# Kernel tuning notes

Hardware: AMD Instinct MI355X
Metric: run time of the kernel (lower is better)

Reference implementation:

```python
import jax, jax.numpy as jnp
from jax import lax
import numpy as np


def conv2d(x, w, b=None, stride=1, pad=0, groups=1):
    out = lax.conv_general_dilated(x, w, (stride, stride), [(pad, pad), (pad, pad)],
                                   dimension_numbers=('NCHW', 'OIHW', 'NCHW'),
                                   feature_group_count=groups)
    if b is not None:
        out = out + b[None, :, None, None]
    return out


def ln(x, g, b, eps=1e-5):
    m = x.mean(-1, keepdims=True)
    v = ((x - m) ** 2).mean(-1, keepdims=True)
    return (x - m) * lax.rsqrt(v + eps) * g + b


def grid_sample_bilinear(img, grid):
    # img [N,C,H,W]; grid [N,Hg,Wg,2] with (x,y) in [-1,1]; align_corners=True, zeros padding
    N, C, H, W = img.shape
    x = (grid[..., 0] + 1.0) * 0.5 * (W - 1)
    y = (grid[..., 1] + 1.0) * 0.5 * (H - 1)
    x0 = jnp.floor(x); y0 = jnp.floor(y)
    x1 = x0 + 1.0; y1 = y0 + 1.0
    wx1 = x - x0; wx0 = 1.0 - wx1
    wy1 = y - y0; wy0 = 1.0 - wy1
    imgh = img.transpose(0, 2, 3, 1)  # [N,H,W,C]
    bidx = jnp.arange(N)[:, None, None]
    def g(ix, iy):
        valid = (ix >= 0) & (ix <= W - 1) & (iy >= 0) & (iy <= H - 1)
        ixc = jnp.clip(ix, 0, W - 1).astype(jnp.int32)
        iyc = jnp.clip(iy, 0, H - 1).astype(jnp.int32)
        return imgh[bidx, iyc, ixc] * valid[..., None].astype(img.dtype)
    out = (g(x0, y0) * (wx0 * wy0)[..., None] + g(x1, y0) * (wx1 * wy0)[..., None]
           + g(x0, y1) * (wx0 * wy1)[..., None] + g(x1, y1) * (wx1 * wy1)[..., None])
    return out.transpose(0, 3, 1, 2)  # [N,C,Hg,Wg]


def setup_inputs() -> dict:
    key = jax.random.key(0)
    ks = iter(jax.random.split(key, 64))
    def rn(shape, s=0.02):
        return jax.random.normal(next(ks), shape, jnp.float32) * s
    B, C, H, W = 4, 512, 32, 32
    gc, hid = 256, 1024
    d = {}
    d['feat_tgt'] = jax.random.normal(next(ks), (B, C, H, W), jnp.float32)
    d['feat_ref'] = jax.random.normal(next(ks), (B, C, H, W), jnp.float32)
    d['emb_w'] = rn((C, 2 * C, 3, 3)); d['emb_b'] = jnp.zeros((C,), jnp.float32)
    d['q_w'] = rn((C, C)); d['q_b'] = jnp.zeros((C,), jnp.float32)
    d['k_w'] = rn((C, C)); d['k_b'] = jnp.zeros((C,), jnp.float32)
    d['v_w'] = rn((C, C)); d['v_b'] = jnp.zeros((C,), jnp.float32)
    d['out_w'] = rn((C, C)); d['out_b'] = jnp.zeros((C,), jnp.float32)
    d['ln1_w'] = jnp.ones((gc,), jnp.float32); d['ln1_b'] = jnp.zeros((gc,), jnp.float32)
    d['mb_n1_w'] = jnp.ones((gc,), jnp.float32); d['mb_n1_b'] = jnp.zeros((gc,), jnp.float32)
    d['mb_q_w'] = rn((gc, gc)); d['mb_q_b'] = jnp.zeros((gc,), jnp.float32)
    d['mb_kv_w'] = rn((2 * gc, gc)); d['mb_kv_b'] = jnp.zeros((2 * gc,), jnp.float32)
    d['mb_proj_w'] = rn((gc, gc)); d['mb_proj_b'] = jnp.zeros((gc,), jnp.float32)
    d['mb_n2_w'] = jnp.ones((gc,), jnp.float32); d['mb_n2_b'] = jnp.zeros((gc,), jnp.float32)
    d['mb_fc1_w'] = rn((hid, gc)); d['mb_fc1_b'] = jnp.zeros((hid,), jnp.float32)
    d['mb_dw_w'] = rn((hid, 1, 3, 3)); d['mb_dw_b'] = jnp.zeros((hid,), jnp.float32)
    d['mb_fc2_w'] = rn((gc, hid)); d['mb_fc2_b'] = jnp.zeros((gc,), jnp.float32)
    d['co_dw_w'] = rn((gc, 1, 9, 9)); d['co_dw_b'] = jnp.zeros((gc,), jnp.float32)
    d['co_ln_w'] = jnp.ones((gc,), jnp.float32); d['co_ln_b'] = jnp.zeros((gc,), jnp.float32)
    d['co_out_w'] = rn((2, gc))
    return d


def reference(feat_tgt, feat_ref, emb_w, emb_b, q_w, q_b, k_w, k_b, v_w, v_b, out_w, out_b,
              ln1_w, ln1_b, mb_n1_w, mb_n1_b, mb_q_w, mb_q_b, mb_kv_w, mb_kv_b,
              mb_proj_w, mb_proj_b, mb_n2_w, mb_n2_b, mb_fc1_w, mb_fc1_b, mb_dw_w, mb_dw_b,
              mb_fc2_w, mb_fc2_b, co_dw_w, co_dw_b, co_ln_w, co_ln_b, co_out_w):
    B, C, H, W = feat_tgt.shape
    G = 2                      # n_groups
    gc = C // G                # n_group_channels
    heads, hc = 8, C // 8      # n_heads, n_head_channels
    # embedding conv over concat(target, reference)
    feat = conv2d(jnp.concatenate([feat_tgt, feat_ref], 1), emb_w, emb_b, pad=1)
    q = jnp.einsum('bchw,oc->bohw', feat_tgt, q_w) + q_b[None, :, None, None]
    # group tokens + LN
    fg = feat.reshape(B * G, gc, H * W).transpose(0, 2, 1)  # [BG, N, gc]
    x = ln(fg, ln1_w, ln1_b)
    # ---- MitBlock offset generator ----
    BG, N, D = x.shape
    mh = 8; mhd = D // mh
    h = ln(x, mb_n1_w, mb_n1_b, 1e-6)
    qq = (h @ mb_q_w.T + mb_q_b).reshape(BG, N, mh, mhd).transpose(0, 2, 1, 3)
    kv = (h @ mb_kv_w.T + mb_kv_b).reshape(BG, N, 2, mh, mhd).transpose(2, 0, 3, 1, 4)
    kk, vv = kv[0], kv[1]
    a = jax.nn.softmax(jnp.einsum('bhnd,bhmd->bhnm', qq, kk) * (mhd ** -0.5), axis=-1)
    o = jnp.einsum('bhnm,bhmd->bhnd', a, vv).transpose(0, 2, 1, 3).reshape(BG, N, D)
    x = x + (o @ mb_proj_w.T + mb_proj_b)
    h2 = ln(x, mb_n2_w, mb_n2_b, 1e-6)
    m = h2 @ mb_fc1_w.T + mb_fc1_b                         # [BG, N, hid]
    hid = m.shape[-1]
    mi = m.transpose(0, 2, 1).reshape(BG, hid, H, W)
    mi = conv2d(mi, mb_dw_w, mb_dw_b, pad=1, groups=hid)
    m = jax.nn.gelu(mi.reshape(BG, hid, N).transpose(0, 2, 1), approximate=False)
    x = x + (m @ mb_fc2_w.T + mb_fc2_b)
    # ---- conv_offset stack ----
    off = x.reshape(BG, H, W, gc).transpose(0, 3, 1, 2)
    off = conv2d(off, co_dw_w, co_dw_b, pad=4, groups=gc)
    off = ln(off.transpose(0, 2, 3, 1), co_ln_w, co_ln_b).transpose(0, 3, 1, 2)
    off = jax.nn.gelu(off, approximate=False)
    off = jnp.einsum('bchw,oc->bohw', off, co_out_w)       # [BG, 2, Hk, Wk]
    Hk, Wk = off.shape[2], off.shape[3]
    ns = Hk * Wk
    rng = jnp.array([1.0 / Hk, 1.0 / Wk], feat.dtype).reshape(1, 2, 1, 1)
    off = jnp.tanh(off) * rng * 2.0                        # offset_range_factor = 2
    off = off.transpose(0, 2, 3, 1)                        # [BG, Hk, Wk, 2] (y,x)
    ry = (jnp.linspace(0.5, Hk - 0.5, Hk, dtype=feat.dtype) / Hk) * 2 - 1
    rx = (jnp.linspace(0.5, Wk - 0.5, Wk, dtype=feat.dtype) / Wk) * 2 - 1
    ref = jnp.stack(jnp.meshgrid(ry, rx, indexing='ij'), -1)  # [Hk, Wk, 2] (y,x)
    pos = off + ref[None]
    sampled = grid_sample_bilinear(feat.reshape(BG, gc, H, W), pos[..., ::-1])
    sampled = sampled.reshape(B, C, ns)
    k = jnp.einsum('bcn,oc->bon', sampled, k_w) + k_b[None, :, None]
    v = jnp.einsum('bcn,oc->bon', sampled, v_w) + v_b[None, :, None]
    qh = q.reshape(B * heads, hc, H * W)
    kh = k.reshape(B * heads, hc, ns)
    vh = v.reshape(B * heads, hc, ns)
    attn = jax.nn.softmax(jnp.einsum('bcm,bcn->bmn', qh, kh) * (hc ** -0.5), axis=-1)
    out = jnp.einsum('bmn,bcn->bcm', attn, vh).reshape(B, C, H, W)
    y = jnp.einsum('bchw,oc->bohw', out, out_w) + out_b[None, :, None, None]
    return y
```

## Files before the change

### kernel.cpp

```cpp
#include <hip/hip_runtime.h>
#include <math.h>


static constexpr int HW = 1024;

typedef __attribute__((ext_vector_type(8))) short bf16x8;
typedef __attribute__((ext_vector_type(4))) float f32x4;

union V16u { int4 i4; ushort u[8]; };

__device__ __forceinline__ float gelu_exact(float v) {
  return 0.5f * v * (1.0f + erff(v * 0.7071067811865475f));
}

__device__ __forceinline__ ushort bf16_rne(float v) {
  unsigned int b = __float_as_uint(v);
  return (ushort)((b + 0x7fffu + ((b >> 16) & 1u)) >> 16);
}

__device__ __forceinline__ void split2(float v, ushort& h, ushort& l) {
  h = bf16_rne(v);
  l = bf16_rne(v - __uint_as_float(((unsigned int)h) << 16));
}

__device__ __forceinline__ void wfrag_body(const float* __restrict__ W, int K, int KC,
                                           ushort* __restrict__ dh, ushort* __restrict__ dl,
                                           int gtid, float scale) {
  int l = gtid & 63; int fr = gtid >> 6;
  int kc = fr % KC; int ot = fr / KC;
  int lr = l & 15, lu = l >> 4;
  const float* sp = W + (size_t)(ot * 16 + lr) * K + kc * 32 + lu * 8;
  V16u hi, lo;
#pragma unroll
  for (int j = 0; j < 8; ++j) split2(sp[j] * scale, hi.u[j], lo.u[j]);
  *(int4*)(dh + (size_t)gtid * 8) = hi.i4;
  *(int4*)(dl + (size_t)gtid * 8) = lo.i4;
}

__global__ void k_prep_all(
    const float* __restrict__ emb_w, const float* __restrict__ tgt,
    const float* __restrict__ refp,
    const float* q_w, const float* k_w, const float* v_w, const float* o_w,
    const float* mq_w, const float* mkv_w, const float* mp_w,
    const float* f1_w, const float* f2_w, const float* dw9_w,
    const float* q_b, const float* mq_b, const float* mkv_b,
    const float* k_b, const float* v_b,
    ushort* __restrict__ WtEH, ushort* __restrict__ WtEL,
    ushort* __restrict__ XtH, ushort* __restrict__ XtL,
    ushort* qh, ushort* ql, ushort* kvh, ushort* kvl,
    ushort* oh, ushort* ol, ushort* mqkvh, ushort* mqkvl,
    ushort* mph, ushort* mpl, ushort* f1h, ushort* f1l, ushort* f2h, ushort* f2l,
    float* wt9, float* biasmb, float* biaskv, float* biasq,
    ushort* tgtfh, ushort* tgtfl) {
  int bid = blockIdx.x, tid = threadIdx.x;
  if (bid < 2048) {
    int idx = bid * 256 + tid;
    int o = idx >> 10, ci = idx & 1023;
    const float* src = emb_w + (size_t)idx * 9;
#pragma unroll
    for (int t = 0; t < 9; ++t) {
      ushort h, l; split2(src[t], h, l);
      size_t oo = ((size_t)(t * 512 + o)) * 1024 + ci;
      WtEH[oo] = h; WtEL[oo] = l;
    }
  } else if (bid < 4360) {
    int idx = (bid - 2048) * 256 + tid;
    int xp = idx % 34; int r = idx / 34;
    int g8 = r & 127; r >>= 7;
    int yp = r % 34; int b = r / 34;
    int y = yp - 1, x = xp - 1;
    bool valid = (unsigned)y < 32u && (unsigned)x < 32u;
    V16u hi, lo;
    const float* in = (g8 < 64) ? (tgt + ((size_t)(b * 512 + g8 * 8)) * HW)
                                : (refp + ((size_t)(b * 512 + (g8 - 64) * 8)) * HW);
#pragma unroll
    for (int j = 0; j < 8; ++j) {
      float v = valid ? in[(size_t)j * HW + y * 32 + x] : 0.f;
      split2(v, hi.u[j], lo.u[j]);
    }
    size_t oo = (((size_t)(b * 34 + yp)) * 34 + xp) * 1024 + g8 * 8;
    *(int4*)(XtH + oo) = hi.i4;
    *(int4*)(XtL + oo) = lo.i4;
  }
  else if (bid < 4488) wfrag_body(q_w, 512, 16, qh, ql, (bid - 4360) * 256 + tid, 0.125f);
  else if (bid < 4616) wfrag_body(k_w, 512, 16, kvh, kvl, (bid - 4488) * 256 + tid, 1.f);
  else if (bid < 4744) wfrag_body(v_w, 512, 16, kvh + 262144, kvl + 262144,
                                  (bid - 4616) * 256 + tid, 1.f);
  else if (bid < 4872) wfrag_body(o_w, 512, 16, oh, ol, (bid - 4744) * 256 + tid, 1.f);
  else if (bid < 4904) wfrag_body(mq_w, 256, 8, mqkvh, mqkvl, (bid - 4872) * 256 + tid,
                                  0.17677669529663689f);
  else if (bid < 4968) wfrag_body(mkv_w, 256, 8, mqkvh + 65536, mqkvl + 65536,
                                  (bid - 4904) * 256 + tid, 1.f);
  else if (bid < 5000) wfrag_body(mp_w, 256, 8, mph, mpl, (bid - 4968) * 256 + tid, 1.f);
  else if (bid < 5128) wfrag_body(f1_w, 256, 8, f1h, f1l, (bid - 5000) * 256 + tid, 1.f);
  else if (bid < 5256) wfrag_body(f2_w, 1024, 32, f2h, f2l, (bid - 5128) * 256 + tid, 1.f);
  else if (bid < 5337) {
    int idx = (bid - 5256) * 256 + tid;
    int t = idx >> 8, c = idx & 255;
    wt9[idx] = dw9_w[c * 81 + t];
  } else if (bid < 5346) {
    int idx = (bid - 5337) * 256 + tid;
    if (idx < 768)
      biasmb[idx] = idx < 256 ? mq_b[idx] * 0.17677669529663689f : mkv_b[idx - 256];
    else if (idx < 1792) {
      int j = idx - 768;
      biaskv[j] = j < 512 ? k_b[j] : v_b[j - 512];
    } else if (idx < 2304) {
      biasq[idx - 1792] = q_b[idx - 1792] * 0.125f;
    }
  } else {
    int gtid = (bid - 5346) * 256 + tid;
    int l = gtid & 63; int fr = gtid >> 6;
    int kc = fr % 16; int r2 = fr / 16; int nt = r2 & 63; int b = r2 >> 6;
    int lr = l & 15, lu = l >> 4;
    const float* sp = tgt + ((size_t)(b * 512) + kc * 32 + lu * 8) * 1024 + nt * 16 + lr;
    V16u hi, lo;
#pragma unroll
    for (int j = 0; j < 8; ++j) split2(sp[(size_t)j * 1024], hi.u[j], lo.u[j]);
    *(int4*)(tgtfh + (size_t)gtid * 8) = hi.i4;
    *(int4*)(tgtfl + (size_t)gtid * 8) = lo.i4;
  }
}

__global__ __launch_bounds__(256, 4)
void k_emb_mfma(const ushort* __restrict__ Xt_hi, const ushort* __restrict__ Xt_lo,
                const ushort* __restrict__ Wt_hi, const ushort* __restrict__ Wt_lo,
                float* __restrict__ part) {
  int wgid = (blockIdx.x & 7) * 128 + (blockIdx.x >> 3);
  int yt = wgid & 7;  wgid >>= 3;
  int b  = wgid & 3;  wgid >>= 2;
  int ks = wgid & 3;  wgid >>= 2;
  int mt = wgid;
  int tid = threadIdx.x;
  int w = tid >> 6, l = tid & 63;
  int lr = l & 15, lu = l >> 4;
  int y0 = yt * 4;
  int obase = mt * 64 + w * 16;

  __shared__ int4 LsH[816];
  __shared__ int4 LsL[816];

  int4 gh[4], gl[4];
  int kc0 = ks * 8;

  auto loadstage = [&](int kcg) {
#pragma unroll
    for (int i = 0; i < 4; ++i) {
      int s = tid + 256 * i;
      if (s < 816) {
        int px = s >> 2;
        int u = (s & 3) ^ ((px >> 1) & 3);
        size_t off = ((size_t)(b * 34 + y0) * 34 + px) * 1024 + kcg * 32 + u * 8;
        gh[i] = *(const int4*)(Xt_hi + off);
        gl[i] = *(const int4*)(Xt_lo + off);
      }
    }
  };
  auto writestage = [&]() {
#pragma unroll
    for (int i = 0; i < 4; ++i) {
      int s = tid + 256 * i;
      if (s < 816) { LsH[s] = gh[i]; LsL[s] = gl[i]; }
    }
  };

  f32x4 zero = {0.f, 0.f, 0.f, 0.f};
  f32x4 acc[8];
#pragma unroll
  for (int n = 0; n < 8; ++n) acc[n] = zero;

  loadstage(kc0);
  writestage();

  for (int kc = 0; kc < 8; ++kc) {
    __syncthreads();
    if (kc < 7) loadstage(kc0 + kc + 1);
    int kcg = kc0 + kc;
    const bf16x8* BH = (const bf16x8*)&LsH[0];
    const bf16x8* BL = (const bf16x8*)&LsL[0];
#pragma unroll
    for (int kx = 0; kx < 3; ++kx) {
      bf16x8 bh[12], bl[12];
#pragma unroll
      for (int f = 0; f < 12; ++f) {
        int px = (f >> 1) * 34 + (f & 1) * 16 + kx + lr;
        int idx = px * 4 + (lu ^ ((px >> 1) & 3));
        bh[f] = BH[idx]; bl[f] = BL[idx];
      }
#pragma unroll
      for (int ky = 0; ky < 3; ++ky) {
        int tap = ky * 3 + kx;
        size_t wo = (((size_t)(tap * 512 + obase + lr)) * 1024) + kcg * 32 + lu * 8;
        bf16x8 ah = *(const bf16x8*)(Wt_hi + wo);
        bf16x8 al = *(const bf16x8*)(Wt_lo + wo);
#pragma unroll
        for (int yr = 0; yr < 4; ++yr)
#pragma unroll
          for (int h = 0; h < 2; ++h) {
            int f = (yr + ky) * 2 + h;
            int nf = yr * 2 + h;
            acc[nf] = __builtin_amdgcn_mfma_f32_16x16x32_bf16(ah, bh[f], acc[nf], 0, 0, 0);
            acc[nf] = __builtin_amdgcn_mfma_f32_16x16x32_bf16(ah, bl[f], acc[nf], 0, 0, 0);
            acc[nf] = __builtin_amdgcn_mfma_f32_16x16x32_bf16(al, bh[f], acc[nf], 0, 0, 0);
          }
      }
    }
    if (kc < 7) {
      __syncthreads();
      writestage();
    }
  }

  float* pb = part + (size_t)ks * 2097152;
#pragma unroll
  for (int yr = 0; yr < 4; ++yr)
#pragma unroll
    for (int h = 0; h < 2; ++h) {
      f32x4 c = acc[yr * 2 + h];
      size_t base = ((size_t)(b * 512 + obase + lu * 4)) * 1024
                    + (y0 + yr) * 32 + h * 16 + lr;
#pragma unroll
      for (int r = 0; r < 4; ++r) pb[base + (size_t)r * 1024] = c[r];
    }
}

__global__ void k_embmerge_nc(const float* __restrict__ part, const float* __restrict__ bias,
                              float* __restrict__ featnc) {
  __shared__ float T[64][65];
  int bid = blockIdx.x;
  int n0 = (bid & 15) << 6; bid >>= 4;
  int c0 = (bid & 3) << 6; int bg = bid >> 2;
  int cl = threadIdx.x & 63, rw = threadIdx.x >> 6;
#pragma unroll
  for (int i = 0; i < 16; ++i) {
    int crow = i * 4 + rw;
    size_t idx = ((size_t)(bg * 256 + c0 + crow)) * 1024 + n0 + cl;
    float v = part[idx] + part[2097152 + idx] + part[4194304 + idx] + part[6291456 + idx];
    T[crow][cl] = v + bias[(bg & 1) * 256 + c0 + crow];
  }
  __syncthreads();
#pragma unroll
  for (int i = 0; i < 16; ++i) {
    int nrow = i * 4 + rw;
    featnc[((size_t)(bg * 1024 + n0 + nrow)) * 256 + c0 + cl] = T[cl][nrow];
  }
}

__global__ __launch_bounds__(256)
void k_gemm_mfma(const ushort* __restrict__ Ah, const ushort* __restrict__ Al,
                 const ushort* __restrict__ Bh, const ushort* __restrict__ Bl,
                 const float* __restrict__ bias, float* __restrict__ Y,
                 int KC, int MT, int Mtot) {
  int bid = blockIdx.x;
  int ntb = bid & 15; bid >>= 4;
  int mt = bid % MT; int b = bid / MT;
  int tid = threadIdx.x, w = tid >> 6, l = tid & 63, lr = l & 15, lu = l >> 4;
  int wo = w >> 1, wn = w & 1;
  int ot0 = mt * 4 + wo * 2;
  int nf0 = ntb * 4 + wn * 2;
  const bf16x8* pAh = (const bf16x8*)Ah;
  const bf16x8* pAl = (const bf16x8*)Al;
  const bf16x8* pBh = (const bf16x8*)Bh;
  const bf16x8* pBl = (const bf16x8*)Bl;
  f32x4 zero = {0.f, 0.f, 0.f, 0.f};
  f32x4 acc[2][2];
#pragma unroll
  for (int a = 0; a < 2; ++a)
#pragma unroll
    for (int n = 0; n < 2; ++n) acc[a][n] = zero;
  for (int kc = 0; kc < KC; ++kc) {
    bf16x8 a_h[2], a_l[2];
#pragma unroll
    for (int a = 0; a < 2; ++a) {
      size_t idx = ((size_t)(ot0 + a) * KC + kc) * 64 + l;
      a_h[a] = pAh[idx]; a_l[a] = pAl[idx];
    }
#pragma unroll
    for (int n = 0; n < 2; ++n) {
      size_t idx = (((size_t)(b * 64 + nf0 + n)) * KC + kc) * 64 + l;
      bf16x8 b_h = pBh[idx], b_l = pBl[idx];
#pragma unroll
      for (int a = 0; a < 2; ++a) {
        acc[a][n] = __builtin_amdgcn_mfma_f32_16x16x32_bf16(a_h[a], b_h, acc[a][n], 0, 0, 0);
        acc[a][n] = __builtin_amdgcn_mfma_f32_16x16x32_bf16(a_h[a], b_l, acc[a][n], 0, 0, 0);
        acc[a][n] = __builtin_amdgcn_mfma_f32_16x16x32_bf16(a_l[a], b_h, acc[a][n], 0, 0, 0);
      }
    }
  }
#pragma unroll
  for (int a = 0; a < 2; ++a) {
    int o = (ot0 + a) * 16 + lu * 4;
#pragma unroll
    for (int n = 0; n < 2; ++n) {
      int col = (nf0 + n) * 16 + lr;
#pragma unroll
      for (int r = 0; r < 4; ++r)
        Y[((size_t)(b * Mtot + o + r)) * 1024 + col] = acc[a][n][r] + bias[o + r];
    }
  }
}

__global__ __launch_bounds__(256)
void k_gemm_resadd(const ushort* __restrict__ Ah, const ushort* __restrict__ Al,
                   const ushort* __restrict__ Bh, const ushort* __restrict__ Bl,
                   const float* __restrict__ bias, const float* __restrict__ res,
                   float* __restrict__ dst, int KC, int MT, int addmode) {
  int bid = blockIdx.x;
  int ntb = bid & 15; bid >>= 4;
  int mt = bid % MT; int b = bid / MT;
  int tid = threadIdx.x, w = tid >> 6, l = tid & 63, lr = l & 15, lu = l >> 4;
  int wo = w >> 1, wn = w & 1;
  int ot0 = mt * 4 + wo * 2;
  int nf0 = ntb * 4 + wn * 2;
  const bf16x8* pAh = (const bf16x8*)Ah;
  const bf16x8* pAl = (const bf16x8*)Al;
  const bf16x8* pBh = (const bf16x8*)Bh;
  const bf16x8* pBl = (const bf16x8*)Bl;
  f32x4 zero = {0.f, 0.f, 0.f, 0.f};
  f32x4 acc[2][2];
#pragma unroll
  for (int a = 0; a < 2; ++a)
#pragma unroll
    for (int n = 0; n < 2; ++n) acc[a][n] = zero;
  for (int kc = 0; kc < KC; ++kc) {
    bf16x8 a_h[2], a_l[2];
#pragma unroll
    for (int a = 0; a < 2; ++a) {
      size_t idx = ((size_t)(ot0 + a) * KC + kc) * 64 + l;
      a_h[a] = pAh[idx]; a_l[a] = pAl[idx];
    }
#pragma unroll
    for (int n = 0; n < 2; ++n) {
      size_t idx = (((size_t)(b * 64 + nf0 + n)) * KC + kc) * 64 + l;
      bf16x8 b_h = pBh[idx], b_l = pBl[idx];
#pragma unroll
      for (int a = 0; a < 2; ++a) {
        acc[a][n] = __builtin_amdgcn_mfma_f32_16x16x32_bf16(a_h[a], b_h, acc[a][n], 0, 0, 0);
        acc[a][n] = __builtin_amdgcn_mfma_f32_16x16x32_bf16(a_h[a], b_l, acc[a][n], 0, 0, 0);
        acc[a][n] = __builtin_amdgcn_mfma_f32_16x16x32_bf16(a_l[a], b_h, acc[a][n], 0, 0, 0);
      }
    }
  }
#pragma unroll
  for (int a = 0; a < 2; ++a) {
    int o = (ot0 + a) * 16 + lu * 4;
#pragma unroll
    for (int n = 0; n < 2; ++n) {
      int col = (nf0 + n) * 16 + lr;
      size_t addr = ((size_t)((b << 10) + col)) * 256 + o;
      float4 v;
      v.x = acc[a][n][0] + bias[o + 0];
      v.y = acc[a][n][1] + bias[o + 1];
      v.z = acc[a][n][2] + bias[o + 2];
      v.w = acc[a][n][3] + bias[o + 3];
      float4 r4 = addmode ? *(const float4*)(dst + addr) : *(const float4*)(res + addr);
      v.x += r4.x; v.y += r4.y; v.z += r4.z; v.w += r4.w;
      *(float4*)(dst + addr) = v;
    }
  }
}

__global__ __launch_bounds__(256)
void k_gemm_frag_mb(const ushort* __restrict__ Ah, const ushort* __restrict__ Al,
                    const ushort* __restrict__ Bh, const ushort* __restrict__ Bl,
                    const float* __restrict__ bias,
                    ushort* __restrict__ mQh, ushort* __restrict__ mQl,
                    ushort* __restrict__ mKh, ushort* __restrict__ mKl,
                    ushort* __restrict__ mVh, ushort* __restrict__ mVl) {
  int bid = blockIdx.x;
  int ntb = bid & 15; bid >>= 4;
  int mt = bid % 12; int b = bid / 12;
  int tid = threadIdx.x, w = tid >> 6, l = tid & 63, lr = l & 15, lu = l >> 4;
  int wo = w >> 1, wn = w & 1;
  int ot0 = mt * 4 + wo * 2;
  int nf0 = ntb * 4 + wn * 2;
  const bf16x8* pAh = (const bf16x8*)Ah;
  const bf16x8* pAl = (const bf16x8*)Al;
  const bf16x8* pBh = (const bf16x8*)Bh;
  const bf16x8* pBl = (const bf16x8*)Bl;
  f32x4 zero = {0.f, 0.f, 0.f, 0.f};
  f32x4 acc[2][2];
#pragma unroll
  for (int a = 0; a < 2; ++a)
#pragma unroll
    for (int n = 0; n < 2; ++n) acc[a][n] = zero;
  for (int kc = 0; kc < 8; ++kc) {
    bf16x8 a_h[2], a_l[2];
#pragma unroll
    for (int a = 0; a < 2; ++a) {
      size_t idx = ((size_t)(ot0 + a) * 8 + kc) * 64 + l;
      a_h[a] = pAh[idx]; a_l[a] = pAl[idx];
    }
#pragma unroll
    for (int n = 0; n < 2; ++n) {
      size_t idx = (((size_t)(b * 64 + nf0 + n)) * 8 + kc) * 64 + l;
      bf16x8 b_h = pBh[idx], b_l = pBl[idx];
#pragma unroll
      for (int a = 0; a < 2; ++a) {
        acc[a][n] = __builtin_amdgcn_mfma_f32_16x16x32_bf16(a_h[a], b_h, acc[a][n], 0, 0, 0);
        acc[a][n] = __builtin_amdgcn_mfma_f32_16x16x32_bf16(a_h[a], b_l, acc[a][n], 0, 0, 0);
        acc[a][n] = __builtin_amdgcn_mfma_f32_16x16x32_bf16(a_l[a], b_h, acc[a][n], 0, 0, 0);
      }
    }
  }
#pragma unroll
  for (int a = 0; a < 2; ++a) {
    int o0 = (ot0 + a) * 16 + lu * 4;
#pragma unroll
    for (int n = 0; n < 2; ++n) {
      int col = (nf0 + n) * 16 + lr;
      ushort4 h4, l4;
      split2(acc[a][n][0] + bias[o0 + 0], h4.x, l4.x);
      split2(acc[a][n][1] + bias[o0 + 1], h4.y, l4.y);
      split2(acc[a][n][2] + bias[o0 + 2], h4.z, l4.z);
      split2(acc[a][n][3] + bias[o0 + 3], h4.w, l4.w);
      if (o0 < 512) {
        int oo = o0 & 255;
        int hh = oo >> 5, d = oo & 31;
        ushort* dh = o0 < 256 ? mQh : mKh;
        ushort* dl = o0 < 256 ? mQl : mKl;
        size_t base = ((((size_t)(b * 8 + hh) * 64 + (col >> 4)) * 64)
                       + ((d >> 3) << 4) + (col & 15)) * 8 + (d & 7);
        *(ushort4*)(dh + base) = h4;
        *(ushort4*)(dl + base) = l4;
      } else {
        int oo = o0 - 512;
        int hh = oo >> 5, d = oo & 31;
        int et = d >> 4;
        size_t eb = ((((size_t)((b * 8 + hh) * 2 + et)) * 32 + (col >> 5)) * 64
                     + ((col >> 3) & 3) * 16 + (d & 15)) * 8 + (col & 7);
        mVh[eb] = h4.x; mVh[eb + 8] = h4.y; mVh[eb + 16] = h4.z; mVh[eb + 24] = h4.w;
        mVl[eb] = l4.x; mVl[eb + 8] = l4.y; mVl[eb + 16] = l4.z; mVl[eb + 24] = l4.w;
      }
    }
  }
}

__global__ __launch_bounds__(256)
void k_gemm_frag_main(const ushort* __restrict__ Ah, const ushort* __restrict__ Al,
                      const ushort* __restrict__ Bh, const ushort* __restrict__ Bl,
                      const float* __restrict__ bias,
                      ushort* __restrict__ fh, ushort* __restrict__ fl,
                      ushort* __restrict__ vfh, ushort* __restrict__ vfl,
                      int vbase, int KC, int MT) {
  int bid = blockIdx.x;
  int ntb = bid & 15; bid >>= 4;
  int mt = bid % MT; int b = bid / MT;
  int tid = threadIdx.x, w = tid >> 6, l = tid & 63, lr = l & 15, lu = l >> 4;
  int wo = w >> 1, wn = w & 1;
  int ot0 = mt * 4 + wo * 2;
  int nf0 = ntb * 4 + wn * 2;
  const bf16x8* pAh = (const bf16x8*)Ah;
  const bf16x8* pAl = (const bf16x8*)Al;
  const bf16x8* pBh = (const bf16x8*)Bh;
  const bf16x8* pBl = (const bf16x8*)Bl;
  f32x4 zero = {0.f, 0.f, 0.f, 0.f};
  f32x4 acc[2][2];
#pragma unroll
  for (int a = 0; a < 2; ++a)
#pragma unroll
    for (int n = 0; n < 2; ++n) acc[a][n] = zero;
  for (int kc = 0; kc < KC; ++kc) {
    bf16x8 a_h[2], a_l[2];
#pragma unroll
    for (int a = 0; a < 2; ++a) {
      size_t idx = ((size_t)(ot0 + a) * KC + kc) * 64 + l;
      a_h[a] = pAh[idx]; a_l[a] = pAl[idx];
    }
#pragma unroll
    for (int n = 0; n < 2; ++n) {
      size_t idx = (((size_t)(b * 64 + nf0 + n)) * KC + kc) * 64 + l;
      bf16x8 b_h = pBh[idx], b_l = pBl[idx];
#pragma unroll
      for (int a = 0; a < 2; ++a) {
        acc[a][n] = __builtin_amdgcn_mfma_f32_16x16x32_bf16(a_h[a], b_h, acc[a][n], 0, 0, 0);
        acc[a][n] = __builtin_amdgcn_mfma_f32_16x16x32_bf16(a_h[a], b_l, acc[a][n], 0, 0, 0);
        acc[a][n] = __builtin_amdgcn_mfma_f32_16x16x32_bf16(a_l[a], b_h, acc[a][n], 0, 0, 0);
      }
    }
  }
#pragma unroll
  for (int a = 0; a < 2; ++a) {
    int o0 = (ot0 + a) * 16 + lu * 4;
#pragma unroll
    for (int n = 0; n < 2; ++n) {
      int col = (nf0 + n) * 16 + lr;
      ushort4 h4, l4;
      split2(acc[a][n][0] + bias[o0 + 0], h4.x, l4.x);
      split2(acc[a][n][1] + bias[o0 + 1], h4.y, l4.y);
      split2(acc[a][n][2] + bias[o0 + 2], h4.z, l4.z);
      split2(acc[a][n][3] + bias[o0 + 3], h4.w, l4.w);
      if (o0 < vbase) {
        int h = o0 >> 6, d = o0 & 63;
        int dc = d >> 5;
        size_t base = (((((size_t)(b * 8 + h) * 64 + (col >> 4)) * 2 + dc) * 64)
                       + (((d & 31) >> 3) << 4) + (col & 15)) * 8 + (d & 7);
        *(ushort4*)(fh + base) = h4;
        *(ushort4*)(fl + base) = l4;
      } else {
        int oo = o0 - vbase;
        int h = oo >> 6, d = oo & 63;
        int et = d >> 4;
        size_t eb = ((((size_t)((b * 8 + h) * 4 + et)) * 32 + (col >> 5)) * 64
                     + ((col >> 3) & 3) * 16 + (d & 15)) * 8 + (col & 7);
        vfh[eb] = h4.x; vfh[eb + 8] = h4.y; vfh[eb + 16] = h4.z; vfh[eb + 24] = h4.w;
        vfl[eb] = l4.x; vfl[eb + 8] = l4.y; vfl[eb + 16] = l4.z; vfl[eb + 24] = l4.w;
      }
    }
  }
}

__global__ void k_ln1n1(const float* __restrict__ featnc,
                        const float* __restrict__ g1, const float* __restrict__ b1,
                        const float* __restrict__ gn, const float* __restrict__ bn,
                        float* __restrict__ xbuf,
                        ushort* __restrict__ dh, ushort* __restrict__ dl) {
  int token = (blockIdx.x * 256 + threadIdx.x) >> 6;
  int lane = threadIdx.x & 63;
  float4 v4 = *reinterpret_cast<const float4*>(featnc + (size_t)token * 256 + lane * 4);
  float s  = v4.x + v4.y + v4.z + v4.w;
  float s2 = v4.x * v4.x + v4.y * v4.y + v4.z * v4.z + v4.w * v4.w;
#pragma unroll
  for (int off = 32; off; off >>= 1) { s += __shfl_xor(s, off); s2 += __shfl_xor(s2, off); }
  float mean = s * (1.f / 256.f);
  float rstd = rsqrtf(s2 * (1.f / 256.f) - mean * mean + 1e-5f);
  float4 g4 = *reinterpret_cast<const float4*>(g1 + lane * 4);
  float4 b4 = *reinterpret_cast<const float4*>(b1 + lane * 4);
  float4 x;
  x.x = (v4.x - mean) * rstd * g4.x + b4.x;
  x.y = (v4.y - mean) * rstd * g4.y + b4.y;
  x.z = (v4.z - mean) * rstd * g4.z + b4.z;
  x.w = (v4.w - mean) * rstd * g4.w + b4.w;
  *reinterpret_cast<float4*>(xbuf + (size_t)token * 256 + lane * 4) = x;
  float t  = x.x + x.y + x.z + x.w;
  float t2 = x.x * x.x + x.y * x.y + x.z * x.z + x.w * x.w;
#pragma unroll
  for (int off = 32; off; off >>= 1) { t += __shfl_xor(t, off); t2 += __shfl_xor(t2, off); }
  float mean2 = t * (1.f / 256.f);
  float rstd2 = rsqrtf(t2 * (1.f / 256.f) - mean2 * mean2 + 1e-6f);
  float4 gg = *reinterpret_cast<const float4*>(gn + lane * 4);
  float4 bb = *reinterpret_cast<const float4*>(bn + lane * 4);
  ushort4 h4, l4;
  split2((x.x - mean2) * rstd2 * gg.x + bb.x, h4.x, l4.x);
  split2((x.y - mean2) * rstd2 * gg.y + bb.y, h4.y, l4.y);
  split2((x.z - mean2) * rstd2 * gg.z + bb.z, h4.z, l4.z);
  split2((x.w - mean2) * rstd2 * gg.w + bb.w, h4.w, l4.w);
  int bg = token >> 10, nt = (token >> 4) & 63, lr = token & 15;
  int kc = lane >> 3, lu_f = (lane >> 1) & 3, j0 = (lane & 1) * 4;
  size_t base = ((((size_t)(bg * 64 + nt)) * 8 + kc) * 64 + lu_f * 16 + lr) * 8 + j0;
  *(ushort4*)(dh + base) = h4;
  *(ushort4*)(dl + base) = l4;
}

__global__ void k_ln_frag(const float* __restrict__ xin, const float* __restrict__ g_,
                          const float* __restrict__ b_, ushort* __restrict__ dh,
                          ushort* __restrict__ dl, float eps) {
  int token = (blockIdx.x * 256 + threadIdx.x) >> 6;
  int lane = threadIdx.x & 63;
  float4 v4 = *reinterpret_cast<const float4*>(xin + (size_t)token * 256 + lane * 4);
  float s  = v4.x + v4.y + v4.z + v4.w;
  float s2 = v4.x * v4.x + v4.y * v4.y + v4.z * v4.z + v4.w * v4.w;
#pragma unroll
  for (int off = 32; off; off >>= 1) { s += __shfl_xor(s, off); s2 += __shfl_xor(s2, off); }
  float mean = s * (1.f / 256.f);
  float rstd = rsqrtf(s2 * (1.f / 256.f) - mean * mean + eps);
  float4 g4 = *reinterpret_cast<const float4*>(g_ + lane * 4);
  float4 b4 = *reinterpret_cast<const float4*>(b_ + lane * 4);
  ushort4 h4, l4;
  split2((v4.x - mean) * rstd * g4.x + b4.x, h4.x, l4.x);
  split2((v4.y - mean) * rstd * g4.y + b4.y, h4.y, l4.y);
  split2((v4.z - mean) * rstd * g4.z + b4.z, h4.z, l4.z);
  split2((v4.w - mean) * rstd * g4.w + b4.w, h4.w, l4.w);
  int bg = token >> 10, nt = (token >> 4) & 63, lr = token & 15;
  int kc = lane >> 3, lu_f = (lane >> 1) & 3, j0 = (lane & 1) * 4;
  size_t base = ((((size_t)(bg * 64 + nt)) * 8 + kc) * 64 + lu_f * 16 + lr) * 8 + j0;
  *(ushort4*)(dh + base) = h4;
  *(ushort4*)(dl + base) = l4;
}

__global__ __launch_bounds__(256)
void k_mbattn_mfma(const ushort* __restrict__ Qh, const ushort* __restrict__ Ql,
                   const ushort* __restrict__ Kh, const ushort* __restrict__ Kl,
                   const ushort* __restrict__ Vh, const ushort* __restrict__ Vl,
                   ushort* __restrict__ ofh, ushort* __restrict__ ofl) {
  int qb = blockIdx.x & 15, bgh = blockIdx.x >> 4;
  int tid = threadIdx.x, w = tid >> 6, l = tid & 63, lr = l & 15, lu = l >> 4;
  int qt = qb * 4 + w;
  bf16x8 qh = ((const bf16x8*)Qh)[(size_t)(bgh * 64 + qt) * 64 + l];
  bf16x8 ql = ((const bf16x8*)Ql)[(size_t)(bgh * 64 + qt) * 64 + l];
  __shared__ ushort Ph[4][16][72];
  __shared__ ushort Pl[4][16][72];
  f32x4 zero = {0.f, 0.f, 0.f, 0.f};
  f32x4 oacc[2] = {zero, zero};
  float den = 0.f;
  for (int kb = 0; kb < 16; ++kb) {
#pragma unroll
    for (int kt4 = 0; kt4 < 4; ++kt4) {
      int kt = kb * 4 + kt4;
      bf16x8 kh = ((const bf16x8*)Kh)[(size_t)(bgh * 64 + kt) * 64 + l];
      bf16x8 kl = ((const bf16x8*)Kl)[(size_t)(bgh * 64 + kt) * 64 + l];
      f32x4 s = zero;
      s = __builtin_amdgcn_mfma_f32_16x16x32_bf16(kh, qh, s, 0, 0, 0);
      s = __builtin_amdgcn_mfma_f32_16x16x32_bf16(kh, ql, s, 0, 0, 0);
      s = __builtin_amdgcn_mfma_f32_16x16x32_bf16(kl, qh, s, 0, 0, 0);
      uint2 uh, ul;
      {
        float p0 = __expf(s[0]), p1 = __expf(s[1]), p2 = __expf(s[2]), p3 = __expf(s[3]);
        den += (p0 + p1) + (p2 + p3);
        ushort h0, l0, h1, l1, h2, l2, h3, l3;
        split2(p0, h0, l0); split2(p1, h1, l1); split2(p2, h2, l2); split2(p3, h3, l3);
        uh.x = (unsigned)h0 | ((unsigned)h1 << 16); uh.y = (unsigned)h2 | ((unsigned)h3 << 16);
        ul.x = (unsigned)l0 | ((unsigned)l1 << 16); ul.y = (unsigned)l2 | ((unsigned)l3 << 16);
      }
      *(uint2*)&Ph[w][lr][kt4 * 16 + lu * 4] = uh;
      *(uint2*)&Pl[w][lr][kt4 * 16 + lu * 4] = ul;
    }
#pragma unroll
    for (int kc2 = 0; kc2 < 2; ++kc2) {
      int kc = kb * 2 + kc2;
      bf16x8 bph = *(const bf16x8*)&Ph[w][lr][kc2 * 32 + lu * 8];
      bf16x8 bpl = *(const bf16x8*)&Pl[w][lr][kc2 * 32 + lu * 8];
#pragma unroll
      for (int et = 0; et < 2; ++et) {
        bf16x8 vh = ((const bf16x8*)Vh)[(size_t)((bgh * 2 + et) * 32 + kc) * 64 + l];
        bf16x8 vl = ((const bf16x8*)Vl)[(size_t)((bgh * 2 + et) * 32 + kc) * 64 + l];
        oacc[et] = __builtin_amdgcn_mfma_f32_16x16x32_bf16(vh, bph, oacc[et], 0, 0, 0);
        oacc[et] = __builtin_amdgcn_mfma_f32_16x16x32_bf16(vh, bpl, oacc[et], 0, 0, 0);
        oacc[et] = __builtin_amdgcn_mfma_f32_16x16x32_bf16(vl, bph, oacc[et], 0, 0, 0);
      }
    }
  }
  den += __shfl_xor(den, 16);
  den += __shfl_xor(den, 32);
  float inv = 1.f / den;
  int bg = bgh >> 3, hh = bgh & 7;
#pragma unroll
  for (int et = 0; et < 2; ++et) {
    ushort4 h4, l4;
    split2(oacc[et][0] * inv, h4.x, l4.x); split2(oacc[et][1] * inv, h4.y, l4.y);
    split2(oacc[et][2] * inv, h4.z, l4.z); split2(oacc[et][3] * inv, h4.w, l4.w);
    int lu_f = et * 2 + (lu >> 1), j0 = (lu & 1) * 4;
    size_t base = ((((size_t)(bg * 64 + qt)) * 8 + hh) * 64 + lu_f * 16 + lr) * 8 + j0;
    *(ushort4*)(ofh + base) = h4;
    *(ushort4*)(ofl + base) = l4;
  }
}

__global__ __launch_bounds__(256)
void k_mainattn_mfma(const ushort* __restrict__ Qh, const ushort* __restrict__ Ql,
                     const ushort* __restrict__ Kh, const ushort* __restrict__ Kl,
                     const ushort* __restrict__ Vh, const ushort* __restrict__ Vl,
                     ushort* __restrict__ anfh, ushort* __restrict__ anfl) {
  int qb = blockIdx.x & 15, bh = blockIdx.x >> 4;
  int tid = threadIdx.x, w = tid >> 6, l = tid & 63, lr = l & 15, lu = l >> 4;
  int qt = qb * 4 + w;
  bf16x8 qh[2], ql[2];
#pragma unroll
  for (int dc = 0; dc < 2; ++dc) {
    qh[dc] = ((const bf16x8*)Qh)[(size_t)((bh * 64 + qt) * 2 + dc) * 64 + l];
    ql[dc] = ((const bf16x8*)Ql)[(size_t)((bh * 64 + qt) * 2 + dc) * 64 + l];
  }
  __shared__ ushort Ph[4][16][72];
  __shared__ ushort Pl[4][16][72];
  f32x4 zero = {0.f, 0.f, 0.f, 0.f};
  f32x4 oacc[4] = {zero, zero, zero, zero};
  float den = 0.f;
  for (int kb = 0; kb < 16; ++kb) {
#pragma unroll
    for (int kt4 = 0; kt4 < 4; ++kt4) {
      int kt = kb * 4 + kt4;
      f32x4 s = zero;
#pragma unroll
      for (int dc = 0; dc < 2; ++dc) {
        bf16x8 kh = ((const bf16x8*)Kh)[(size_t)((bh * 64 + kt) * 2 + dc) * 64 + l];
        bf16x8 kl = ((const bf16x8*)Kl)[(size_t)((bh * 64 + kt) * 2 + dc) * 64 + l];
        s = __builtin_amdgcn_mfma_f32_16x16x32_bf16(kh, qh[dc], s, 0, 0, 0);
        s = __builtin_amdgcn_mfma_f32_16x16x32_bf16(kh, ql[dc], s, 0, 0, 0);
        s = __builtin_amdgcn_mfma_f32_16x16x32_bf16(kl, qh[dc], s, 0, 0, 0);
      }
      uint2 uh, ul;
      {
        float p0 = __expf(s[0]), p1 = __expf(s[1]), p2 = __expf(s[2]), p3 = __expf(s[3]);
        den += (p0 + p1) + (p2 + p3);
        ushort h0, l0, h1, l1, h2, l2, h3, l3;
        split2(p0, h0, l0); split2(p1, h1, l1); split2(p2, h2, l2); split2(p3, h3, l3);
        uh.x = (unsigned)h0 | ((unsigned)h1 << 16); uh.y = (unsigned)h2 | ((unsigned)h3 << 16);
        ul.x = (unsigned)l0 | ((unsigned)l1 << 16); ul.y = (unsigned)l2 | ((unsigned)l3 << 16);
      }
      *(uint2*)&Ph[w][lr][kt4 * 16 + lu * 4] = uh;
      *(uint2*)&Pl[w][lr][kt4 * 16 + lu * 4] = ul;
    }
#pragma unroll
    for (int kc2 = 0; kc2 < 2; ++kc2) {
      int kc = kb * 2 + kc2;
      bf16x8 bph = *(const bf16x8*)&Ph[w][lr][kc2 * 32 + lu * 8];
      bf16x8 bpl = *(const bf16x8*)&Pl[w][lr][kc2 * 32 + lu * 8];
#pragma unroll
      for (int et = 0; et < 4; ++et) {
        bf16x8 vh = ((const bf16x8*)Vh)[(size_t)((bh * 4 + et) * 32 + kc) * 64 + l];
        bf16x8 vl = ((const bf16x8*)Vl)[(size_t)((bh * 4 + et) * 32 + kc) * 64 + l];
        oacc[et] = __builtin_amdgcn_mfma_f32_16x16x32_bf16(vh, bph, oacc[et], 0, 0, 0);
        oacc[et] = __builtin_amdgcn_mfma_f32_16x16x32_bf16(vh, bpl, oacc[et], 0, 0, 0);
        oacc[et] = __builtin_amdgcn_mfma_f32_16x16x32_bf16(vl, bph, oacc[et], 0, 0, 0);
      }
    }
  }
  den += __shfl_xor(den, 16);
  den += __shfl_xor(den, 32);
  float inv = 1.f / den;
  int b = bh >> 3, h = bh & 7;
#pragma unroll
  for (int et = 0; et < 4; ++et) {
    ushort4 h4, l4;
    split2(oacc[et][0] * inv, h4.x, l4.x); split2(oacc[et][1] * inv, h4.y, l4.y);
    split2(oacc[et][2] * inv, h4.z, l4.z); split2(oacc[et][3] * inv, h4.w, l4.w);
    int kc = h * 2 + (et >> 1);
    int lu_f = (et & 1) * 2 + (lu >> 1), j0 = (lu & 1) * 4;
    size_t base = ((((size_t)(b * 64 + qt)) * 16 + kc) * 64 + lu_f * 16 + lr) * 8 + j0;
    *(ushort4*)(anfh + base) = h4;
    *(ushort4*)(anfl + base) = l4;
  }
}

__global__ void k_dw3_frag(const float* __restrict__ X, const float* __restrict__ w,
                           const float* __restrict__ bias,
                           ushort* __restrict__ dh, ushort* __restrict__ dl) {
  int bid = blockIdx.x;
  int pch = bid & 3; bid >>= 2;
  int chg = bid & 127; int bg = bid >> 7;
  int tid = threadIdx.x;
  int n = pch * 256 + tid;
  int x = n & 31, y = n >> 5;
  int ch0 = chg * 8;
  V16u hi, lo;
#pragma unroll
  for (int jj = 0; jj < 8; ++jj) {
    int ch = ch0 + jj;
    const float* src = X + ((size_t)((bg << 10) + ch)) * HW;
    const float* wr = w + ch * 9;
    float acc = bias[ch];
#pragma unroll
    for (int ky = 0; ky < 3; ++ky) {
      int yy = y + ky - 1;
      if ((unsigned)yy < 32u) {
        const float* row = src + yy * 32;
#pragma unroll
        for (int kx = 0; kx < 3; ++kx) {
          int xx = x + kx - 1;
          if ((unsigned)xx < 32u) acc += row[xx] * wr[ky * 3 + kx];
        }
      }
    }
    split2(gelu_exact(acc), hi.u[jj], lo.u[jj]);
  }
  size_t base = ((((size_t)(bg * 64 + (n >> 4)) * 32 + (ch0 >> 5)) * 64)
                 + ((ch0 >> 3) & 3) * 16 + (n & 15)) * 8;
  *(int4*)(dh + base) = hi.i4;
  *(int4*)(dl + base) = lo.i4;
}

__global__ void k_dw9cotail(const float* __restrict__ Xnc, const float* __restrict__ wt9,
                            const float* __restrict__ bias,
                            const float* __restrict__ lnw, const float* __restrict__ lnb,
                            const float* __restrict__ w2, float* __restrict__ pos) {
  int bid = blockIdx.x;
  int pt = bid & 127; int bg = bid >> 7;
  int tid = threadIdx.x;
  int y = pt >> 2, x0 = (pt & 3) * 8;
  float acc[8];
  float bs = bias[tid];
#pragma unroll
  for (int p = 0; p < 8; ++p) acc[p] = bs;
  const float* src = Xnc + (size_t)(bg << 10) * 256;
  for (int ky = 0; ky < 9; ++ky) {
    int yy = y + ky - 4;
    if ((unsigned)yy >= 32u) continue;
#pragma unroll
    for (int kx = 0; kx < 9; ++kx) {
      float wv = wt9[(ky * 9 + kx) * 256 + tid];
#pragma unroll
      for (int p = 0; p < 8; ++p) {
        int xx = x0 + p + kx - 4;
        if ((unsigned)xx < 32u)
          acc[p] += src[(size_t)(yy * 32 + xx) * 256 + tid] * wv;
      }
    }
  }
  __shared__ float rs[8][4], rs2[8][4], ro0[8][4], ro1[8][4];
  int wv = tid >> 6, ln = tid & 63;
  float lw = lnw[tid], lb = lnb[tid];
  float wa = w2[tid], wb = w2[256 + tid];
#pragma unroll
  for (int p = 0; p < 8; ++p) {
    float a = acc[p], b2 = acc[p] * acc[p];
#pragma unroll
    for (int off = 32; off; off >>= 1) { a += __shfl_xor(a, off); b2 += __shfl_xor(b2, off); }
    if (ln == 0) { rs[p][wv] = a; rs2[p][wv] = b2; }
  }
  __syncthreads();
#pragma unroll
  for (int p = 0; p < 8; ++p) {
    float tot  = rs[p][0] + rs[p][1] + rs[p][2] + rs[p][3];
    float tot2 = rs2[p][0] + rs2[p][1] + rs2[p][2] + rs2[p][3];
    float mean = tot * (1.f / 256.f);
    float rstd = rsqrtf(tot2 * (1.f / 256.f) - mean * mean + 1e-5f);
    float ge = gelu_exact((acc[p] - mean) * rstd * lw + lb);
    float o0 = ge * wa, o1 = ge * wb;
#pragma unroll
    for (int off = 32; off; off >>= 1) { o0 += __shfl_xor(o0, off); o1 += __shfl_xor(o1, off); }
    if (ln == 0) { ro0[p][wv] = o0; ro1[p][wv] = o1; }
  }
  __syncthreads();
  if (tid < 8) {
    int p = tid;
    float o0 = ro0[p][0] + ro0[p][1] + ro0[p][2] + ro0[p][3];
    float o1 = ro1[p][0] + ro1[p][1] + ro1[p][2] + ro1[p][3];
    float offy = tanhf(o0) * (2.f / 32.f);
    float offx = tanhf(o1) * (2.f / 32.f);
    int n = y * 32 + x0 + p;
    float refy = ((y + 0.5f) * (1.f / 32.f)) * 2.f - 1.f;
    float refx = ((x0 + p + 0.5f) * (1.f / 32.f)) * 2.f - 1.f;
    pos[((bg << 10) + n) * 2]     = offx + refx;
    pos[((bg << 10) + n) * 2 + 1] = offy + refy;
  }
}

__global__ void k_gsample_frag(const float* __restrict__ Xnc, const float* __restrict__ pos,
                               ushort* __restrict__ dh, ushort* __restrict__ dl) {
  int bid = blockIdx.x;
  int nch = bid & 15; int bg = bid >> 4;
  int tid = threadIdx.x;
  __shared__ int sI[4][64];
  __shared__ float sW[4][64];
  if (tid < 64) {
    int j = nch * 64 + tid;
    float gx = pos[((bg << 10) + j) * 2];
    float gy = pos[((bg << 10) + j) * 2 + 1];
    float fx = (gx + 1.f) * 0.5f * 31.f;
    float fy = (gy + 1.f) * 0.5f * 31.f;
    float x0f = floorf(fx), y0f = floorf(fy);
    int x0 = (int)x0f, y0 = (int)y0f;
    float wx1 = fx - x0f, wx0 = 1.f - wx1;
    float wy1 = fy - y0f, wy0 = 1.f - wy1;
    bool vx0 = (x0 >= 0) & (x0 <= 31);
    bool vx1 = (x0 + 1 >= 0) & (x0 + 1 <= 31);
    bool vy0 = (y0 >= 0) & (y0 <= 31);
    bool vy1 = (y0 + 1 >= 0) & (y0 + 1 <= 31);
    int cx0 = min(max(x0, 0), 31), cx1 = min(max(x0 + 1, 0), 31);
    int cy0 = min(max(y0, 0), 31), cy1 = min(max(y0 + 1, 0), 31);
    sW[0][tid] = wx0 * wy0 * ((vx0 && vy0) ? 1.f : 0.f);
    sW[1][tid] = wx1 * wy0 * ((vx1 && vy0) ? 1.f : 0.f);
    sW[2][tid] = wx0 * wy1 * ((vx0 && vy1) ? 1.f : 0.f);
    sW[3][tid] = wx1 * wy1 * ((vx1 && vy1) ? 1.f : 0.f);
    sI[0][tid] = cy0 * 32 + cx0; sI[1][tid] = cy0 * 32 + cx1;
    sI[2][tid] = cy1 * 32 + cx0; sI[3][tid] = cy1 * 32 + cx1;
  }
  __syncthreads();
  int b = bg >> 1, g = bg & 1;
  const float* src = Xnc + (size_t)(bg << 10) * 256;
  for (int nn = 0; nn < 64; ++nn) {
    float acc = src[(size_t)sI[0][nn] * 256 + tid] * sW[0][nn]
              + src[(size_t)sI[1][nn] * 256 + tid] * sW[1][nn]
              + src[(size_t)sI[2][nn] * 256 + tid] * sW[2][nn]
              + src[(size_t)sI[3][nn] * 256 + tid] * sW[3][nn];
    ushort h, l; split2(acc, h, l);
    int jglob = nch * 64 + nn;
    size_t addr = ((((size_t)(b * 64 + (jglob >> 4)) * 16) + g * 8 + (tid >> 5)) * 64
                   + ((tid >> 3) & 3) * 16 + (jglob & 15)) * 8 + (tid & 7);
    dh[addr] = h; dl[addr] = l;
  }
}

extern "C" void kernel_launch(void* const* d_in, const int* in_sizes, int n_in,
                              void* d_out, int out_size, void* d_ws, size_t ws_size,
                              hipStream_t stream) {
  const float* tgt    = (const float*)d_in[0];
  const float* refp   = (const float*)d_in[1];
  const float* emb_w  = (const float*)d_in[2];
  const float* emb_b  = (const float*)d_in[3];
  const float* q_w    = (const float*)d_in[4];
  const float* q_b    = (const float*)d_in[5];
  const float* k_w    = (const float*)d_in[6];
  const float* k_b    = (const float*)d_in[7];
  const float* v_w    = (const float*)d_in[8];
  const float* v_b    = (const float*)d_in[9];
  const float* out_w  = (const float*)d_in[10];
  const float* out_b  = (const float*)d_in[11];
  const float* ln1_w  = (const float*)d_in[12];
  const float* ln1_b  = (const float*)d_in[13];
  const float* n1_w   = (const float*)d_in[14];
  const float* n1_b   = (const float*)d_in[15];
  const float* mbq_w  = (const float*)d_in[16];
  const float* mbq_b  = (const float*)d_in[17];
  const float* mbkv_w = (const float*)d_in[18];
  const float* mbkv_b = (const float*)d_in[19];
  const float* mbp_w  = (const float*)d_in[20];
  const float* mbp_b  = (const float*)d_in[21];
  const float* n2_w   = (const float*)d_in[22];
  const float* n2_b   = (const float*)d_in[23];
  const float* fc1_w  = (const float*)d_in[24];
  const float* fc1_b  = (const float*)d_in[25];
  const float* dw3_w  = (const float*)d_in[26];
  const float* dw3_b  = (const float*)d_in[27];
  const float* fc2_w  = (const float*)d_in[28];
  const float* fc2_b  = (const float*)d_in[29];
  const float* dw9_w  = (const float*)d_in[30];
  const float* dw9_b  = (const float*)d_in[31];
  const float* coln_w = (const float*)d_in[32];
  const float* coln_b = (const float*)d_in[33];
  const float* coout_w= (const float*)d_in[34];

  float* ws = (float*)d_ws;
  float* slabA = ws + 0;
  float* qfrag = ws + 2097152;
  float* xbuf  = ws + 4194304;
  float* slabF = ws + 10485760;
  float* slabG = ws + 14680064;
  float* slabH = ws + 23068672;
  float* featnc= ws + 31457280;
  float* posb  = ws + 35389440;
  float* wt9   = ws + 35405824;
  float* biasmb= ws + 35426560;
  float* biaskv= ws + 35427328;
  float* biasq = ws + 35428352;

  ushort* XtH = (ushort*)(ws + 4194304);
  ushort* XtL = XtH + 4734976;
  ushort* WtEH = (ushort*)slabG;
  ushort* WtEL = WtEH + 4718592;
  float* part = slabH;
  ushort* tgtfh = (ushort*)slabF;
  ushort* tgtfl = tgtfh + 2097152;

  ushort* J = (ushort*)(ws + 33554432);
  ushort* wfq_h   = J;                ushort* wfq_l   = J + 262144;
  ushort* wfkv_h  = J + 524288;       ushort* wfkv_l  = J + 1048576;
  ushort* wfo_h   = J + 1572864;      ushort* wfo_l   = J + 1835008;
  ushort* wfmqkv_h= J + 2097152;      ushort* wfmqkv_l= J + 2293760;
  ushort* wfmp_h  = J + 2490368;      ushort* wfmp_l  = J + 2555904;
  ushort* wff1_h  = J + 2621440;      ushort* wff1_l  = J + 2883584;
  ushort* wff2_h  = J + 3145728;      ushort* wff2_l  = J + 3407872;

  ushort* hfh = (ushort*)slabH;     ushort* hfl = hfh + 2097152;
  ushort* mQh = (ushort*)slabG;     ushort* mQl = mQh + 2097152;
  ushort* mKh = mQh + 4194304;      ushort* mKl = mQh + 6291456;
  ushort* mVh = mQh + 8388608;      ushort* mVl = mQh + 10485760;
  ushort* ofh = (ushort*)slabF;     ushort* ofl = ofh + 2097152;
  ushort* h2fh = (ushort*)slabF;    ushort* h2fl = h2fh + 2097152;
  float* m_cm = slabG;
  ushort* mifh = (ushort*)slabH;    ushort* mifl = mifh + 8388608;
  float* offin = slabA;
  ushort* sfh = (ushort*)slabF;     ushort* sfl = sfh + 2097152;
  ushort* aQh = (ushort*)qfrag;     ushort* aQl = aQh + 2097152;
  ushort* aKh = (ushort*)slabG;     ushort* aKl = aKh + 2097152;
  ushort* aVh = aKh + 4194304;      ushort* aVl = aKh + 6291456;
  ushort* anfh = (ushort*)slabH;    ushort* anfl = anfh + 2097152;

  k_prep_all<<<6370, 256, 0, stream>>>(
      emb_w, tgt, refp, q_w, k_w, v_w, out_w, mbq_w, mbkv_w, mbp_w, fc1_w, fc2_w,
      dw9_w, q_b, mbq_b, mbkv_b, k_b, v_b,
      WtEH, WtEL, XtH, XtL,
      wfq_h, wfq_l, wfkv_h, wfkv_l, wfo_h, wfo_l, wfmqkv_h, wfmqkv_l,
      wfmp_h, wfmp_l, wff1_h, wff1_l, wff2_h, wff2_l,
      wt9, biasmb, biaskv, biasq, tgtfh, tgtfl);
  k_emb_mfma<<<1024, 256, 0, stream>>>(XtH, XtL, WtEH, WtEL, part);
  k_embmerge_nc<<<512, 256, 0, stream>>>(part, emb_b, featnc);
  k_gemm_frag_main<<<512, 256, 0, stream>>>(wfq_h, wfq_l, tgtfh, tgtfl, biasq,
                                            aQh, aQl, aVh, aVl, 512, 16, 8);
  k_ln1n1<<<2048, 256, 0, stream>>>(featnc, ln1_w, ln1_b, n1_w, n1_b, xbuf, hfh, hfl);
  k_gemm_frag_mb<<<1536, 256, 0, stream>>>(wfmqkv_h, wfmqkv_l, hfh, hfl, biasmb,
                                           mQh, mQl, mKh, mKl, mVh, mVl);
  k_mbattn_mfma<<<1024, 256, 0, stream>>>(mQh, mQl, mKh, mKl, mVh, mVl, ofh, ofl);
  k_gemm_resadd<<<512, 256, 0, stream>>>(wfmp_h, wfmp_l, ofh, ofl, mbp_b,
                                         xbuf, xbuf, 8, 4, 1);
  k_ln_frag<<<2048, 256, 0, stream>>>(xbuf, n2_w, n2_b, h2fh, h2fl, 1e-6f);
  k_gemm_mfma<<<2048, 256, 0, stream>>>(wff1_h, wff1_l, h2fh, h2fl, fc1_b, m_cm, 8, 16, 1024);
  k_dw3_frag<<<4096, 256, 0, stream>>>(m_cm, dw3_w, dw3_b, mifh, mifl);
  k_gemm_resadd<<<512, 256, 0, stream>>>(wff2_h, wff2_l, mifh, mifl, fc2_b,
                                         xbuf, offin, 32, 4, 0);
  k_dw9cotail<<<1024, 256, 0, stream>>>(offin, wt9, dw9_b, coln_w, coln_b, coout_w, posb);
  k_gsample_frag<<<128, 256, 0, stream>>>(featnc, posb, sfh, sfl);
  k_gemm_frag_main<<<1024, 256, 0, stream>>>(wfkv_h, wfkv_l, sfh, sfl, biaskv,
                                             aKh, aKl, aVh, aVl, 512, 16, 16);
  k_mainattn_mfma<<<512, 256, 0, stream>>>(aQh, aQl, aKh, aKl, aVh, aVl, anfh, anfl);
  k_gemm_mfma<<<512, 256, 0, stream>>>(wfo_h, wfo_l, anfh, anfl, out_b, (float*)d_out, 16, 8, 512);
}
```

Before: 630.2 us.

## Double output-channel tile in embedding conv GEMM and double-buffer LDS stages

The embedding 3x3 conv MFMA kernel now computes 32 output channels per wave instead of 16. Each LDS-loaded input fragment is reused across two weight fragments, which halves the grid and the number of LDS input loads per output. LDS staging becomes double-buffered, so the second barrier per K-chunk is removed. In exchange the accumulator registers double and launch bounds drop to 2 blocks per SM, which lowers occupancy.

```diff
diff --git a/kernel.cpp b/kernel.cpp
--- a/kernel.cpp
+++ b/kernel.cpp
@@ -122,23 +122,23 @@
   }
 }
 
-__global__ __launch_bounds__(256, 4)
+__global__ __launch_bounds__(256, 2)
 void k_emb_mfma(const ushort* __restrict__ Xt_hi, const ushort* __restrict__ Xt_lo,
                 const ushort* __restrict__ Wt_hi, const ushort* __restrict__ Wt_lo,
                 float* __restrict__ part) {
-  int wgid = (blockIdx.x & 7) * 128 + (blockIdx.x >> 3);
+  int wgid = (blockIdx.x & 7) * 64 + (blockIdx.x >> 3);
   int yt = wgid & 7;  wgid >>= 3;
   int b  = wgid & 3;  wgid >>= 2;
-  int ks = wgid & 3;  wgid >>= 2;
-  int mt = wgid;
+  int mt = wgid & 3;  wgid >>= 2;
+  int ks = wgid;
   int tid = threadIdx.x;
   int w = tid >> 6, l = tid & 63;
   int lr = l & 15, lu = l >> 4;
   int y0 = yt * 4;
-  int obase = mt * 64 + w * 16;
-
-  __shared__ int4 LsH[816];
-  __shared__ int4 LsL[816];
+  int obase = mt * 128 + w * 32;
+
+  __shared__ int4 LsH[2][816];
+  __shared__ int4 LsL[2][816];
 
   int4 gh[4], gl[4];
   int kc0 = ks * 8;
@@ -156,28 +156,31 @@
       }
     }
   };
-  auto writestage = [&]() {
+  auto writestage = [&](int buf) {
 #pragma unroll
     for (int i = 0; i < 4; ++i) {
       int s = tid + 256 * i;
-      if (s < 816) { LsH[s] = gh[i]; LsL[s] = gl[i]; }
+      if (s < 816) { LsH[buf][s] = gh[i]; LsL[buf][s] = gl[i]; }
     }
   };
 
   f32x4 zero = {0.f, 0.f, 0.f, 0.f};
-  f32x4 acc[8];
-#pragma unroll
-  for (int n = 0; n < 8; ++n) acc[n] = zero;
+  f32x4 acc[2][8];
+#pragma unroll
+  for (int a = 0; a < 2; ++a)
+#pragma unroll
+    for (int n = 0; n < 8; ++n) acc[a][n] = zero;
 
   loadstage(kc0);
-  writestage();
+  writestage(0);
 
   for (int kc = 0; kc < 8; ++kc) {
+    int buf = kc & 1;
     __syncthreads();
     if (kc < 7) loadstage(kc0 + kc + 1);
     int kcg = kc0 + kc;
-    const bf16x8* BH = (const bf16x8*)&LsH[0];
-    const bf16x8* BL = (const bf16x8*)&LsL[0];
+    const bf16x8* BH = (const bf16x8*)&LsH[buf][0];
+    const bf16x8* BL = (const bf16x8*)&LsL[buf][0];
 #pragma unroll
     for (int kx = 0; kx < 3; ++kx) {
       bf16x8 bh[12], bl[12];
@@ -191,37 +194,41 @@
       for (int ky = 0; ky < 3; ++ky) {
         int tap = ky * 3 + kx;
         size_t wo = (((size_t)(tap * 512 + obase + lr)) * 1024) + kcg * 32 + lu * 8;
-        bf16x8 ah = *(const bf16x8*)(Wt_hi + wo);
-        bf16x8 al = *(const bf16x8*)(Wt_lo + wo);
+        bf16x8 ah0 = *(const bf16x8*)(Wt_hi + wo);
+        bf16x8 al0 = *(const bf16x8*)(Wt_lo + wo);
+        bf16x8 ah1 = *(const bf16x8*)(Wt_hi + wo + 16 * 1024);
+        bf16x8 al1 = *(const bf16x8*)(Wt_lo + wo + 16 * 1024);
 #pragma unroll
         for (int yr = 0; yr < 4; ++yr)
 #pragma unroll
           for (int h = 0; h < 2; ++h) {
             int f = (yr + ky) * 2 + h;
             int nf = yr * 2 + h;
-            acc[nf] = __builtin_amdgcn_mfma_f32_16x16x32_bf16(ah, bh[f], acc[nf], 0, 0, 0);
-            acc[nf] = __builtin_amdgcn_mfma_f32_16x16x32_bf16(ah, bl[f], acc[nf], 0, 0, 0);
-            acc[nf] = __builtin_amdgcn_mfma_f32_16x16x32_bf16(al, bh[f], acc[nf], 0, 0, 0);
+            acc[0][nf] = __builtin_amdgcn_mfma_f32_16x16x32_bf16(ah0, bh[f], acc[0][nf], 0, 0, 0);
+            acc[0][nf] = __builtin_amdgcn_mfma_f32_16x16x32_bf16(ah0, bl[f], acc[0][nf], 0, 0, 0);
+            acc[0][nf] = __builtin_amdgcn_mfma_f32_16x16x32_bf16(al0, bh[f], acc[0][nf], 0, 0, 0);
+            acc[1][nf] = __builtin_amdgcn_mfma_f32_16x16x32_bf16(ah1, bh[f], acc[1][nf], 0, 0, 0);
+            acc[1][nf] = __builtin_amdgcn_mfma_f32_16x16x32_bf16(ah1, bl[f], acc[1][nf], 0, 0, 0);
+            acc[1][nf] = __builtin_amdgcn_mfma_f32_16x16x32_bf16(al1, bh[f], acc[1][nf], 0, 0, 0);
           }
       }
     }
-    if (kc < 7) {
-      __syncthreads();
-      writestage();
-    }
+    if (kc < 7) writestage(buf ^ 1);
   }
 
   float* pb = part + (size_t)ks * 2097152;
 #pragma unroll
-  for (int yr = 0; yr < 4; ++yr)
-#pragma unroll
-    for (int h = 0; h < 2; ++h) {
-      f32x4 c = acc[yr * 2 + h];
-      size_t base = ((size_t)(b * 512 + obase + lu * 4)) * 1024
-                    + (y0 + yr) * 32 + h * 16 + lr;
-#pragma unroll
-      for (int r = 0; r < 4; ++r) pb[base + (size_t)r * 1024] = c[r];
-    }
+  for (int a = 0; a < 2; ++a)
+#pragma unroll
+    for (int yr = 0; yr < 4; ++yr)
+#pragma unroll
+      for (int h = 0; h < 2; ++h) {
+        f32x4 c = acc[a][yr * 2 + h];
+        size_t base = ((size_t)(b * 512 + obase + a * 16 + lu * 4)) * 1024
+                      + (y0 + yr) * 32 + h * 16 + lr;
+#pragma unroll
+        for (int r = 0; r < 4; ++r) pb[base + (size_t)r * 1024] = c[r];
+      }
 }
 
 __global__ void k_embmerge_nc(const float* __restrict__ part, const float* __restrict__ bias,
@@ -963,7 +970,7 @@
       wfq_h, wfq_l, wfkv_h, wfkv_l, wfo_h, wfo_l, wfmqkv_h, wfmqkv_l,
       wfmp_h, wfmp_l, wff1_h, wff1_l, wff2_h, wff2_l,
       wt9, biasmb, biaskv, biasq, tgtfh, tgtfl);
-  k_emb_mfma<<<1024, 256, 0, stream>>>(XtH, XtL, WtEH, WtEL, part);
+  k_emb_mfma<<<512, 256, 0, stream>>>(XtH, XtL, WtEH, WtEL, part);
   k_embmerge_nc<<<512, 256, 0, stream>>>(part, emb_b, featnc);
   k_gemm_frag_main<<<512, 256, 0, stream>>>(wfq_h, wfq_l, tgtfh, tgtfl, biasq,
                                             aQh, aQl, aVh, aVl, 512, 16, 8);
```

Result: faster. 545.6 us (-13.4%).
